# Kernel optimization log

Measured on AMD Instinct MI355X. Metric: run time of the kernel, lower is better.

## Reference

```python
import jax, jax.numpy as jnp
import numpy as np

B, T, K, D = 32, 1000, 512, 512


def setup_inputs() -> dict:
    key = jax.random.key(0)
    ks = jax.random.split(key, 10)
    s = lambda k, shape: jax.random.normal(k, shape, jnp.float32) * 0.05
    return {
        "zi": jax.random.randint(ks[0], (B, T), 0, K),
        "c": jax.random.normal(ks[1], (B, D, T), jnp.float32),
        "emb": s(ks[2], (K, D)),
        "W1": s(ks[3], (2 * D, D)), "b1": jnp.zeros((D,), jnp.float32),
        "W2": s(ks[4], (D, D)), "b2": jnp.zeros((D,), jnp.float32),
        "W_ih": s(ks[5], (D, 4 * D)), "b_ih": jnp.zeros((4 * D,), jnp.float32),
        "W_hh": s(ks[6], (D, 4 * D)), "b_hh": jnp.zeros((4 * D,), jnp.float32),
        "W_out": s(ks[7], (D, K)), "b_out": jnp.zeros((K,), jnp.float32),
    }


def reference(zi, c, emb, W1, b1, W2, b2, W_ih, b_ih, W_hh, b_hh, W_out, b_out):
    Bb, Tt = zi.shape
    Dd = emb.shape[1]
    # teacher-forced inputs: embed and shift right by one (pad with zeros)
    z = emb[zi]                                                    # [B,T,D]
    z_prev = jnp.concatenate([jnp.zeros((Bb, 1, Dd), z.dtype), z[:, :-1]], axis=1)
    x = jnp.concatenate([z_prev, jnp.transpose(c, (0, 2, 1))], axis=-1)  # [B,T,2D]
    # prenet has no sequential dependence -> batch over all timesteps
    pre = jax.nn.relu(x @ W1 + b1) @ W2 + b2                       # [B,T,D]
    # precompute the input-to-hidden gate contribution for all steps
    xg = jnp.transpose(pre @ W_ih + b_ih + b_hh, (1, 0, 2))        # [T,B,4D]

    def step(carry, gx):
        h, cc = carry
        gates = gx + h @ W_hh                                      # [B,4D]
        i, f, g, o = jnp.split(gates, 4, axis=-1)                  # torch LSTMCell order
        i = jax.nn.sigmoid(i)
        f = jax.nn.sigmoid(f)
        g = jnp.tanh(g)
        o = jax.nn.sigmoid(o)
        cc = f * cc + i * g
        h = o * jnp.tanh(cc)
        return (h, cc), h

    h0 = jnp.zeros((Bb, Dd), pre.dtype)
    _, hs = jax.lax.scan(step, (h0, h0), xg)                       # [T,B,D]
    logits = hs @ W_out + b_out                                    # [T,B,K]
    return jnp.transpose(logits, (1, 2, 0))                        # [B,K,T]
```

## Files before the change

### kernel.cpp

```cpp
#include <hip/hip_runtime.h>
#include <stdint.h>

typedef unsigned short u16;
typedef unsigned int u32;
typedef unsigned long long u64;
typedef __attribute__((ext_vector_type(8))) short bh8;
typedef __attribute__((ext_vector_type(8))) unsigned short u16x8;
typedef __attribute__((ext_vector_type(4))) float f32x4;
typedef __attribute__((ext_vector_type(4))) unsigned int u32x4;

#define B_ 32
#define T_ 1000
#define D_ 512
#define NG 2048

__device__ __forceinline__ float bf2f(u16 u) {
  union { unsigned int i; float f; } v; v.i = ((unsigned int)u) << 16; return v.f;
}
__device__ __forceinline__ u16 f2bf(float f) {
  union { float f; unsigned int i; } v; v.f = f;
  return (u16)((v.i + 0x7fffu + ((v.i >> 16) & 1u)) >> 16);
}

__global__ __launch_bounds__(256) void wtrans_k(const float* __restrict__ src,
                                                u16* __restrict__ dst, int R, int C) {
  __shared__ float tile[32][33];
  const int r0 = blockIdx.x * 32, c0 = blockIdx.y * 32;
  const int tid = threadIdx.x;
#pragma unroll
  for (int q = 0; q < 4; q++) {
    int idx = q * 256 + tid, rr = idx >> 5, cc = idx & 31;
    tile[rr][cc] = src[(size_t)(r0 + rr) * C + c0 + cc];
  }
  __syncthreads();
#pragma unroll
  for (int q = 0; q < 4; q++) {
    int idx = q * 256 + tid, cc = idx >> 5, rr = idx & 31;
    dst[(size_t)(c0 + cc) * R + r0 + rr] = f2bf(tile[rr][cc]);
  }
}

__global__ void bsum_k(const float* __restrict__ a, const float* __restrict__ b,
                       float* __restrict__ o) {
  int i = blockIdx.x * blockDim.x + threadIdx.x;
  if (i < NG) o[i] = a[i] + b[i];
}

__global__ __launch_bounds__(256) void embed_k(const int* __restrict__ zi,
                                               const float* __restrict__ emb,
                                               u16* __restrict__ x) {
  const int tid = threadIdx.x;
  const int r = blockIdx.x * 4 + (tid >> 6);
  const int d0 = (tid & 63) * 8;
  const int t = r >> 5, b = r & 31;
  u16x8 o;
  if (t == 0) {
#pragma unroll
    for (int i = 0; i < 8; i++) o[i] = 0;
  } else {
    const int zv = zi[b * T_ + t - 1];
    const float* s = emb + (size_t)zv * D_ + d0;
#pragma unroll
    for (int i = 0; i < 8; i++) o[i] = f2bf(s[i]);
  }
  *(u16x8*)(x + (size_t)r * 1024 + d0) = o;
}

__global__ __launch_bounds__(256) void ctrans_k(const float* __restrict__ c,
                                                u16* __restrict__ x) {
  __shared__ float tile[32][65];
  const int b = blockIdx.z, d0 = blockIdx.y * 32, t0 = blockIdx.x * 64;
  const int tid = threadIdx.x;
  const int dd = tid >> 3, tt0 = (tid & 7) * 8;
  const float* src = c + ((size_t)b * D_ + d0 + dd) * T_ + t0 + tt0;
#pragma unroll
  for (int i = 0; i < 8; i++) {
    int tt = tt0 + i;
    tile[dd][tt] = (t0 + tt < T_) ? src[i] : 0.f;
  }
  __syncthreads();
  const int tt = tid & 63, dq = tid >> 6;
  if (t0 + tt < T_) {
    u16x8 o;
#pragma unroll
    for (int i = 0; i < 8; i++) o[i] = f2bf(tile[dq * 8 + i][tt]);
    *(u16x8*)(x + ((size_t)(t0 + tt) * 32 + b) * 1024 + 512 + d0 + dq * 8) = o;
  }
}

template <bool RELU, bool SCATTER>
__global__ __launch_bounds__(256, 2) void gemm_k(const u16* __restrict__ A,
                                                 const u16* __restrict__ Bt,
                                                 const float* __restrict__ bias,
                                                 void* __restrict__ Cout,
                                                 int M, int N, int K) {
  __shared__ u16 Al[128 * 40];
  __shared__ u16 Bl[128 * 40];
  const int tid = threadIdx.x;
  const int w = tid >> 6, l = tid & 63;
  const int row0 = blockIdx.x * 128, col0 = blockIdx.y * 128;
  const int wr = (w >> 1) * 64, wc = (w & 1) * 64;
  f32x4 acc[4][4];
  const f32x4 zero = {0.f, 0.f, 0.f, 0.f};
#pragma unroll
  for (int i = 0; i < 4; i++)
#pragma unroll
    for (int j = 0; j < 4; j++) acc[i][j] = zero;

  const int sm = tid >> 2;
  const int sk = (tid & 3) * 8;
  const u16* Ap = A + (size_t)(row0 + sm) * K + sk;
  const u16* Bp = Bt + (size_t)(col0 + sm) * K + sk;
  const size_t half = (size_t)64 * K;
  const int ldo = sm * 40 + sk;
  const int lr = l & 15, lk = (l >> 4) * 8;
  const int KT = K >> 5;

  bh8 a0 = *(const bh8*)Ap, a1 = *(const bh8*)(Ap + half);
  bh8 b0 = *(const bh8*)Bp, b1 = *(const bh8*)(Bp + half);

  for (int kt = 0; kt < KT; kt++) {
    const int kn = (kt + 1 < KT) ? (kt + 1) * 32 : 0;
    bh8 na0 = *(const bh8*)(Ap + kn), na1 = *(const bh8*)(Ap + half + kn);
    bh8 nb0 = *(const bh8*)(Bp + kn), nb1 = *(const bh8*)(Bp + half + kn);
    *(bh8*)(Al + ldo) = a0;
    *(bh8*)(Al + ldo + 64 * 40) = a1;
    *(bh8*)(Bl + ldo) = b0;
    *(bh8*)(Bl + ldo + 64 * 40) = b1;
    __syncthreads();
    bh8 af[4], bfr[4];
#pragma unroll
    for (int i = 0; i < 4; i++) af[i] = *(const bh8*)(Al + (wr + i * 16 + lr) * 40 + lk);
#pragma unroll
    for (int j = 0; j < 4; j++) bfr[j] = *(const bh8*)(Bl + (wc + j * 16 + lr) * 40 + lk);
#pragma unroll
    for (int i = 0; i < 4; i++)
#pragma unroll
      for (int j = 0; j < 4; j++)
        acc[i][j] = __builtin_amdgcn_mfma_f32_16x16x32_bf16(af[i], bfr[j], acc[i][j], 0, 0, 0);
    __syncthreads();
    a0 = na0; a1 = na1; b0 = nb0; b1 = nb1;
  }

  const int lrow = (l >> 4) * 4;
#pragma unroll
  for (int j = 0; j < 4; j++) {
    const int n = col0 + wc + j * 16 + lr;
    const float bv = bias[n];
#pragma unroll
    for (int i = 0; i < 4; i++) {
      const int r = row0 + wr + i * 16 + lrow;
      if (SCATTER) {
        const int bb = r / T_;
        const int t = r - bb * T_;
        f32x4 o;
#pragma unroll
        for (int e = 0; e < 4; e++) o[e] = acc[i][j][e] + bv;
        *(f32x4*)((float*)Cout + ((size_t)bb * N + n) * T_ + t) = o;
      } else {
#pragma unroll
        for (int e = 0; e < 4; e++) {
          float v = acc[i][j][e] + bv;
          if (RELU) v = v > 0.f ? v : 0.f;
          ((u16*)Cout)[(size_t)(r + e) * N + n] = f2bf(v);
        }
      }
    }
  }
}

__global__ __launch_bounds__(256, 1) void scan_k(const u16* __restrict__ xg,
                                                 const u16* __restrict__ Whht,
                                                 u16* __restrict__ hs,
                                                 u32* hbuf) {
  __shared__ u16 hstage[16 * 552];
  __shared__ float gl[4 * 132];
  const int tid = threadIdx.x;
  const int wgid = blockIdx.x;
  const int grp = wgid & 7;
  const int wgin = wgid >> 3;
  if (wgin >= 16) return;
  const int D0 = wgin * 32;
  const int w = tid >> 6, l = tid & 63;
  const int lr = l & 15, lc = l >> 4;
  const int aoff = lc * 136 + lr * 8;

  u32* fb = hbuf;
  u32* sb = hbuf + 32768;

  bh8 bfr[2][16];
#pragma unroll
  for (int j = 0; j < 2; j++) {
    const int c = w * 512 + D0 + j * 16 + lr;
    const u16* wp = Whht + (size_t)c * 512 + lc * 8;
#pragma unroll
    for (int kk = 0; kk < 16; kk++) bfr[j][kk] = *(const bh8*)(wp + kk * 32);
  }

  for (int i = tid; i < 16 * 552 / 2; i += 256) ((u32*)hstage)[i] = 0u;

  const int pb = tid >> 5, pd = tid & 31;
  const int gbat = grp * 4 + pb;
  const int gdim = D0 + pd;
  float ccv = 0.f;
  u16 xh[4];
  if (tid < 128) {
    const u16* xp = xg + (size_t)gbat * NG + gdim;
#pragma unroll
    for (int g = 0; g < 4; g++) xh[g] = xp[g * 512];
  }
  const int rb = tid >> 6;
  const int rd0 = (tid & 63) * 8;
  const int stidx = (rd0 >> 5) * 552 + ((rd0 >> 3) & 3) * 136 + rb * 8;
  bool slowmode = false;
  __syncthreads();

  for (int t = 0; t < T_; t++) {
    f32x4 a0 = {0.f, 0.f, 0.f, 0.f}, a1 = a0;
#pragma unroll
    for (int kk = 0; kk < 16; kk++) {
      bh8 af = *(const bh8*)(hstage + kk * 552 + aoff);
      a0 = __builtin_amdgcn_mfma_f32_16x16x32_bf16(af, bfr[0][kk], a0, 0, 0, 0);
      a1 = __builtin_amdgcn_mfma_f32_16x16x32_bf16(af, bfr[1][kk], a1, 0, 0, 0);
    }
    if (lc == 0) {
#pragma unroll
      for (int e = 0; e < 4; e++) {
        gl[e * 132 + w * 32 + lr] = a0[e];
        gl[e * 132 + w * 32 + 16 + lr] = a1[e];
      }
    }
    asm volatile("s_waitcnt lgkmcnt(0)\n\ts_barrier" ::: "memory");
    __builtin_amdgcn_sched_barrier(0);

    u16 hb = 0;
    if (tid < 128) {
      const float gi = gl[pb * 132 + pd]      + bf2f(xh[0]);
      const float gf = gl[pb * 132 + 32 + pd] + bf2f(xh[1]);
      const float gg = gl[pb * 132 + 64 + pd] + bf2f(xh[2]);
      const float go = gl[pb * 132 + 96 + pd] + bf2f(xh[3]);
      const float si = 1.f / (1.f + __expf(-gi));
      const float sf = 1.f / (1.f + __expf(-gf));
      const float tg = 1.f - 2.f / (__expf(2.f * gg) + 1.f);
      const float so = 1.f / (1.f + __expf(-go));
      ccv = sf * ccv + si * tg;
      const float hv = so * (1.f - 2.f / (__expf(2.f * ccv) + 1.f));
      hb = f2bf(hv);
      if (t + 1 < T_) {
        const u32 tagged = ((u32)(t + 1) << 16) | (u32)hb;
        const size_t idx = ((size_t)((t & 1) * 8 + grp) * 4 + pb) * 512 + gdim;
        asm volatile("global_store_dword %0, %1, off sc0"
                     :: "v"((u64)(uintptr_t)(fb + idx)), "v"(tagged) : "memory");
        (void)__hip_atomic_exchange(sb + idx, tagged, __ATOMIC_RELAXED,
                                    __HIP_MEMORY_SCOPE_AGENT);
      }
    }
    if (t + 1 < T_) {
      const u32 tag = (u32)(t + 1);
      const size_t base = ((size_t)((t & 1) * 8 + grp) * 4 + rb) * 512 + rd0;
      const u64 pa = (u64)(uintptr_t)(fb + base);
      u32x4 qa, qb;
      if (!slowmode) {
        int rounds = 0;
        for (;;) {
          asm volatile("global_load_dwordx4 %0, %2, off sc0\n\t"
                       "global_load_dwordx4 %1, %2, off offset:16 sc0\n\t"
                       "s_waitcnt vmcnt(0)"
                       : "=&v"(qa), "=&v"(qb) : "v"(pa) : "memory");
          const bool bad = (qa[0] >> 16) != tag || (qa[1] >> 16) != tag ||
                           (qa[2] >> 16) != tag || (qa[3] >> 16) != tag ||
                           (qb[0] >> 16) != tag || (qb[1] >> 16) != tag ||
                           (qb[2] >> 16) != tag || (qb[3] >> 16) != tag;
          if (!__ballot(bad)) break;
          if (++rounds > 512) { slowmode = true; break; }
        }
      }
      if (slowmode) {
        const u64* sp = (const u64*)(sb + base);
        for (;;) {
          u64 s0 = __hip_atomic_load(sp + 0, __ATOMIC_RELAXED, __HIP_MEMORY_SCOPE_AGENT);
          u64 s1 = __hip_atomic_load(sp + 1, __ATOMIC_RELAXED, __HIP_MEMORY_SCOPE_AGENT);
          u64 s2 = __hip_atomic_load(sp + 2, __ATOMIC_RELAXED, __HIP_MEMORY_SCOPE_AGENT);
          u64 s3 = __hip_atomic_load(sp + 3, __ATOMIC_RELAXED, __HIP_MEMORY_SCOPE_AGENT);
          qa[0] = (u32)s0; qa[1] = (u32)(s0 >> 32);
          qa[2] = (u32)s1; qa[3] = (u32)(s1 >> 32);
          qb[0] = (u32)s2; qb[1] = (u32)(s2 >> 32);
          qb[2] = (u32)s3; qb[3] = (u32)(s3 >> 32);
          const bool bad = (qa[0] >> 16) != tag || (qa[1] >> 16) != tag ||
                           (qa[2] >> 16) != tag || (qa[3] >> 16) != tag ||
                           (qb[0] >> 16) != tag || (qb[1] >> 16) != tag ||
                           (qb[2] >> 16) != tag || (qb[3] >> 16) != tag;
          if (!__ballot(bad)) break;
        }
      }
      u32x4 pw;
      pw[0] = (qa[0] & 0xffffu) | (qa[1] << 16);
      pw[1] = (qa[2] & 0xffffu) | (qa[3] << 16);
      pw[2] = (qb[0] & 0xffffu) | (qb[1] << 16);
      pw[3] = (qb[2] & 0xffffu) | (qb[3] << 16);
      *(u32x4*)(hstage + stidx) = pw;
    }
    if (tid < 128) {
      hs[((size_t)gbat * T_ + t) * 512 + gdim] = hb;
      if (t + 1 < T_) {
        const u16* xp = xg + ((size_t)(t + 1) * 32 + gbat) * NG + gdim;
#pragma unroll
        for (int g = 0; g < 4; g++) xh[g] = xp[g * 512];
      }
    }
    asm volatile("s_waitcnt lgkmcnt(0)\n\ts_barrier" ::: "memory");
    __builtin_amdgcn_sched_barrier(0);
  }
}

extern "C" void kernel_launch(void* const* d_in, const int* in_sizes, int n_in,
                              void* d_out, int out_size, void* d_ws, size_t ws_size,
                              hipStream_t stream) {
  const int*   zi    = (const int*)d_in[0];
  const float* c     = (const float*)d_in[1];
  const float* emb   = (const float*)d_in[2];
  const float* W1    = (const float*)d_in[3];
  const float* b1    = (const float*)d_in[4];
  const float* W2    = (const float*)d_in[5];
  const float* b2    = (const float*)d_in[6];
  const float* W_ih  = (const float*)d_in[7];
  const float* b_ih  = (const float*)d_in[8];
  const float* W_hh  = (const float*)d_in[9];
  const float* b_hh  = (const float*)d_in[10];
  const float* W_out = (const float*)d_in[11];
  const float* b_out = (const float*)d_in[12];
  float* out = (float*)d_out;
  char* ws = (char*)d_ws;

  const size_t x_off   = 0;
  const size_t xg_off  = 65536000;
  const size_t pre_off = 32768000;
  const size_t w_off   = xg_off + 131072000;
  u16* xb    = (u16*)(ws + x_off);
  u16* hsb   = (u16*)(ws + x_off);
  u16* preb  = (u16*)(ws + pre_off);
  u16* xgb   = (u16*)(ws + xg_off);
  u16* h1b   = (u16*)(ws + xg_off);
  u16* W1t   = (u16*)(ws + w_off);
  u16* W2t   = W1t + 512 * 1024;
  u16* Wiht  = W2t + 512 * 512;
  u16* Whht  = Wiht + 2048 * 512;
  u16* Woutt = Whht + 2048 * 512;
  float* bsum = (float*)(Woutt + 512 * 512);
  u32* hbuf  = (u32*)(bsum + NG);

  hipMemsetAsync(hbuf, 0, 2 * 32768 * sizeof(u32), stream);

  wtrans_k<<<dim3(32, 16), 256, 0, stream>>>(W1, W1t, 1024, 512);
  wtrans_k<<<dim3(16, 16), 256, 0, stream>>>(W2, W2t, 512, 512);
  wtrans_k<<<dim3(16, 64), 256, 0, stream>>>(W_ih, Wiht, 512, 2048);
  wtrans_k<<<dim3(16, 64), 256, 0, stream>>>(W_hh, Whht, 512, 2048);
  wtrans_k<<<dim3(16, 16), 256, 0, stream>>>(W_out, Woutt, 512, 512);
  bsum_k<<<8, 256, 0, stream>>>(b_ih, b_hh, bsum);
  embed_k<<<8000, 256, 0, stream>>>(zi, emb, xb);
  ctrans_k<<<dim3(16, 16, 32), 256, 0, stream>>>(c, xb);

  gemm_k<true,  false><<<dim3(250, 4),  256, 0, stream>>>(xb,   W1t,   b1,    h1b,  32000, 512,  1024);
  gemm_k<false, false><<<dim3(250, 4),  256, 0, stream>>>(h1b,  W2t,   b2,    preb, 32000, 512,  512);
  gemm_k<false, false><<<dim3(250, 16), 256, 0, stream>>>(preb, Wiht,  bsum,  xgb,  32000, 2048, 512);
  scan_k<<<256, 256, 0, stream>>>(xgb, Whht, hsb, hbuf);
  gemm_k<false, true ><<<dim3(250, 4),  256, 0, stream>>>(hsb,  Woutt, b_out, out,  32000, 512,  512);
}
```

Before: 2.970 ms.

## Split gate and polling warps, keep W_hh fragments in AGPRs via inline MFMA

Result: slower. 3.488 ms (+17.4%).

```diff
diff --git a/kernel.cpp b/kernel.cpp
--- a/kernel.cpp
+++ b/kernel.cpp
@@ -188,13 +188,15 @@
   u32* fb = hbuf;
   u32* sb = hbuf + 32768;
 
-  bh8 bfr[2][16];
-#pragma unroll
-  for (int j = 0; j < 2; j++) {
-    const int c = w * 512 + D0 + j * 16 + lr;
-    const u16* wp = Whht + (size_t)c * 512 + lc * 8;
-#pragma unroll
-    for (int kk = 0; kk < 16; kk++) bfr[j][kk] = *(const bh8*)(wp + kk * 32);
+  bh8 bfr0[16], bfr1[16];
+  {
+    const u16* wp0 = Whht + (size_t)(w * 512 + D0 + lr) * 512 + lc * 8;
+    const u16* wp1 = Whht + (size_t)(w * 512 + D0 + 16 + lr) * 512 + lc * 8;
+#pragma unroll
+    for (int kk = 0; kk < 16; kk++) {
+      bfr0[kk] = *(const bh8*)(wp0 + kk * 32);
+      bfr1[kk] = *(const bh8*)(wp1 + kk * 32);
+    }
   }
 
   for (int i = tid; i < 16 * 552 / 2; i += 256) ((u32*)hstage)[i] = 0u;
@@ -209,8 +211,9 @@
 #pragma unroll
     for (int g = 0; g < 4; g++) xh[g] = xp[g * 512];
   }
-  const int rb = tid >> 6;
-  const int rd0 = (tid & 63) * 8;
+  const int rtid = tid - 128;
+  const int rb = rtid >> 5;
+  const int rd0 = (rtid & 31) * 16;
   const int stidx = (rd0 >> 5) * 552 + ((rd0 >> 3) & 3) * 136 + rb * 8;
   bool slowmode = false;
   __syncthreads();
@@ -220,9 +223,12 @@
 #pragma unroll
     for (int kk = 0; kk < 16; kk++) {
       bh8 af = *(const bh8*)(hstage + kk * 552 + aoff);
-      a0 = __builtin_amdgcn_mfma_f32_16x16x32_bf16(af, bfr[0][kk], a0, 0, 0, 0);
-      a1 = __builtin_amdgcn_mfma_f32_16x16x32_bf16(af, bfr[1][kk], a1, 0, 0, 0);
-    }
+      asm("v_mfma_f32_16x16x32_bf16 %0, %2, %3, %0\n\t"
+          "v_mfma_f32_16x16x32_bf16 %1, %2, %4, %1"
+          : "+v"(a0), "+v"(a1)
+          : "v"(af), "a"(bfr0[kk]), "a"(bfr1[kk]));
+    }
+    asm volatile("s_nop 7\n\ts_nop 7\n\ts_nop 7" : "+v"(a0), "+v"(a1));
     if (lc == 0) {
 #pragma unroll
       for (int e = 0; e < 4; e++) {
@@ -233,7 +239,6 @@
     asm volatile("s_waitcnt lgkmcnt(0)\n\ts_barrier" ::: "memory");
     __builtin_amdgcn_sched_barrier(0);
 
-    u16 hb = 0;
     if (tid < 128) {
       const float gi = gl[pb * 132 + pd]      + bf2f(xh[0]);
       const float gf = gl[pb * 132 + 32 + pd] + bf2f(xh[1]);
@@ -245,7 +250,7 @@
       const float so = 1.f / (1.f + __expf(-go));
       ccv = sf * ccv + si * tg;
       const float hv = so * (1.f - 2.f / (__expf(2.f * ccv) + 1.f));
-      hb = f2bf(hv);
+      const u16 hb = f2bf(hv);
       if (t + 1 < T_) {
         const u32 tagged = ((u32)(t + 1) << 16) | (u32)hb;
         const size_t idx = ((size_t)((t & 1) * 8 + grp) * 4 + pb) * 512 + gdim;
@@ -254,59 +259,64 @@
         (void)__hip_atomic_exchange(sb + idx, tagged, __ATOMIC_RELAXED,
                                     __HIP_MEMORY_SCOPE_AGENT);
       }
-    }
-    if (t + 1 < T_) {
+      hs[((size_t)gbat * T_ + t) * 512 + gdim] = hb;
+      if (t + 1 < T_) {
+        const u16* xp = xg + ((size_t)(t + 1) * 32 + gbat) * NG + gdim;
+#pragma unroll
+        for (int g = 0; g < 4; g++) xh[g] = xp[g * 512];
+      }
+    } else if (t + 1 < T_) {
       const u32 tag = (u32)(t + 1);
       const size_t base = ((size_t)((t & 1) * 8 + grp) * 4 + rb) * 512 + rd0;
       const u64 pa = (u64)(uintptr_t)(fb + base);
-      u32x4 qa, qb;
+      u32x4 q0, q1, q2, q3;
       if (!slowmode) {
         int rounds = 0;
         for (;;) {
-          asm volatile("global_load_dwordx4 %0, %2, off sc0\n\t"
-                       "global_load_dwordx4 %1, %2, off offset:16 sc0\n\t"
+          asm volatile("global_load_dwordx4 %0, %4, off sc0\n\t"
+                       "global_load_dwordx4 %1, %4, off offset:16 sc0\n\t"
+                       "global_load_dwordx4 %2, %4, off offset:32 sc0\n\t"
+                       "global_load_dwordx4 %3, %4, off offset:48 sc0\n\t"
                        "s_waitcnt vmcnt(0)"
-                       : "=&v"(qa), "=&v"(qb) : "v"(pa) : "memory");
-          const bool bad = (qa[0] >> 16) != tag || (qa[1] >> 16) != tag ||
-                           (qa[2] >> 16) != tag || (qa[3] >> 16) != tag ||
-                           (qb[0] >> 16) != tag || (qb[1] >> 16) != tag ||
-                           (qb[2] >> 16) != tag || (qb[3] >> 16) != tag;
-          if (!__ballot(bad)) break;
+                       : "=&v"(q0), "=&v"(q1), "=&v"(q2), "=&v"(q3) : "v"(pa) : "memory");
+          u32 bad = 0;
+#pragma unroll
+          for (int e = 0; e < 4; e++)
+            bad |= (q0[e] >> 16) ^ tag | (q1[e] >> 16) ^ tag |
+                   (q2[e] >> 16) ^ tag | (q3[e] >> 16) ^ tag;
+          if (!__ballot(bad != 0u)) break;
           if (++rounds > 512) { slowmode = true; break; }
         }
       }
       if (slowmode) {
         const u64* sp = (const u64*)(sb + base);
         for (;;) {
-          u64 s0 = __hip_atomic_load(sp + 0, __ATOMIC_RELAXED, __HIP_MEMORY_SCOPE_AGENT);
-          u64 s1 = __hip_atomic_load(sp + 1, __ATOMIC_RELAXED, __HIP_MEMORY_SCOPE_AGENT);
-          u64 s2 = __hip_atomic_load(sp + 2, __ATOMIC_RELAXED, __HIP_MEMORY_SCOPE_AGENT);
-          u64 s3 = __hip_atomic_load(sp + 3, __ATOMIC_RELAXED, __HIP_MEMORY_SCOPE_AGENT);
-          qa[0] = (u32)s0; qa[1] = (u32)(s0 >> 32);
-          qa[2] = (u32)s1; qa[3] = (u32)(s1 >> 32);
-          qb[0] = (u32)s2; qb[1] = (u32)(s2 >> 32);
-          qb[2] = (u32)s3; qb[3] = (u32)(s3 >> 32);
-          const bool bad = (qa[0] >> 16) != tag || (qa[1] >> 16) != tag ||
-                           (qa[2] >> 16) != tag || (qa[3] >> 16) != tag ||
-                           (qb[0] >> 16) != tag || (qb[1] >> 16) != tag ||
-                           (qb[2] >> 16) != tag || (qb[3] >> 16) != tag;
-          if (!__ballot(bad)) break;
+          u32x4 v[4];
+#pragma unroll
+          for (int i = 0; i < 8; i++) {
+            u64 s = __hip_atomic_load(sp + i, __ATOMIC_RELAXED, __HIP_MEMORY_SCOPE_AGENT);
+            v[i >> 1][(i & 1) * 2] = (u32)s;
+            v[i >> 1][(i & 1) * 2 + 1] = (u32)(s >> 32);
+          }
+          u32 bad = 0;
+#pragma unroll
+          for (int i = 0; i < 4; i++)
+#pragma unroll
+            for (int e = 0; e < 4; e++) bad |= (v[i][e] >> 16) ^ tag;
+          if (!__ballot(bad != 0u)) { q0 = v[0]; q1 = v[1]; q2 = v[2]; q3 = v[3]; break; }
         }
       }
-      u32x4 pw;
-      pw[0] = (qa[0] & 0xffffu) | (qa[1] << 16);
-      pw[1] = (qa[2] & 0xffffu) | (qa[3] << 16);
-      pw[2] = (qb[0] & 0xffffu) | (qb[1] << 16);
-      pw[3] = (qb[2] & 0xffffu) | (qb[3] << 16);
-      *(u32x4*)(hstage + stidx) = pw;
-    }
-    if (tid < 128) {
-      hs[((size_t)gbat * T_ + t) * 512 + gdim] = hb;
-      if (t + 1 < T_) {
-        const u16* xp = xg + ((size_t)(t + 1) * 32 + gbat) * NG + gdim;
-#pragma unroll
-        for (int g = 0; g < 4; g++) xh[g] = xp[g * 512];
-      }
+      u32x4 w0, w1;
+      w0[0] = (q0[0] & 0xffffu) | (q0[1] << 16);
+      w0[1] = (q0[2] & 0xffffu) | (q0[3] << 16);
+      w0[2] = (q1[0] & 0xffffu) | (q1[1] << 16);
+      w0[3] = (q1[2] & 0xffffu) | (q1[3] << 16);
+      w1[0] = (q2[0] & 0xffffu) | (q2[1] << 16);
+      w1[1] = (q2[2] & 0xffffu) | (q2[3] << 16);
+      w1[2] = (q3[0] & 0xffffu) | (q3[1] << 16);
+      w1[3] = (q3[2] & 0xffffu) | (q3[3] << 16);
+      *(u32x4*)(hstage + stidx) = w0;
+      *(u32x4*)(hstage + stidx + 136) = w1;
     }
     asm volatile("s_waitcnt lgkmcnt(0)\n\ts_barrier" ::: "memory");
     __builtin_amdgcn_sched_barrier(0);
```
